# Kernel tuning notes

Hardware: AMD Instinct MI355X
Metric: run time of the kernel (lower is better)

## Reference

```python
import jax, jax.numpy as jnp
import numpy as np

N, E, D, H, L, R = 10000, 48000, 768, 4, 4, 3
NEG = -1e30


def setup_inputs() -> dict:
    key = jax.random.key(0)
    ks = jax.random.split(key, 16)
    s = 0.02
    return {
        'node_features': jax.random.normal(ks[0], (N, D), jnp.float32),
        'edge_index': jax.random.randint(ks[1], (2, E), 0, N, jnp.int64 if jax.config.jax_enable_x64 else jnp.int32),
        'edge_type': jax.random.randint(ks[2], (E,), 0, R, jnp.int64 if jax.config.jax_enable_x64 else jnp.int32),
        'rel_W': jax.random.normal(ks[3], (R, D, D), jnp.float32) * s,
        'rel_b': jnp.zeros((R, D), jnp.float32),
        'gat_W': jax.random.normal(ks[4], (L, D, H * D), jnp.float32) * s,
        'gat_att_src': jax.random.normal(ks[5], (L, H, D), jnp.float32) * s,
        'gat_att_dst': jax.random.normal(ks[6], (L, H, D), jnp.float32) * s,
        'gat_bias': jnp.zeros((L, D), jnp.float32),
        'proj_W1': jax.random.normal(ks[7], (D, 512), jnp.float32) * s,
        'proj_b1': jnp.zeros((512,), jnp.float32),
        'proj_W2': jax.random.normal(ks[8], (512, D), jnp.float32) * s,
        'proj_b2': jnp.zeros((D,), jnp.float32),
    }


def _gat_rel(g, a_src, a_dst, bias, src, dst, emask):
    # g: [N,H,D] transformed per-head node features; PyG GATConv with
    # add_self_loops=True, leaky_relu slope 0.2, concat=False (head mean).
    alpha_s = jnp.einsum('nhd,hd->nh', g, a_src)   # [N,H]
    alpha_d = jnp.einsum('nhd,hd->nh', g, a_dst)   # [N,H]
    e = jax.nn.leaky_relu(alpha_s[src] + alpha_d[dst], 0.2)  # [E,H]
    e = jnp.where(emask[:, None], e, NEG)          # mask other relations
    e_self = jax.nn.leaky_relu(alpha_s + alpha_d, 0.2)       # [N,H] self loops
    m = jax.ops.segment_max(e, dst, num_segments=N)
    m = jnp.maximum(m, e_self)                     # stable softmax max per dst
    p = jnp.where(emask[:, None], jnp.exp(e - m[dst]), 0.0)  # [E,H]
    p_self = jnp.exp(e_self - m)                   # [N,H]
    denom = jax.ops.segment_sum(p, dst, num_segments=N) + p_self
    msg = jax.ops.segment_sum(p[:, :, None] * g[src], dst, num_segments=N)
    msg = msg + p_self[:, :, None] * g             # [N,H,D]
    out = msg / denom[:, :, None]
    return out.mean(axis=1) + bias                 # concat=False -> head mean


def reference(node_features, edge_index, edge_type, rel_W, rel_b, gat_W,
              gat_att_src, gat_att_dst, gat_bias, proj_W1, proj_b1,
              proj_W2, proj_b2):
    src, dst = edge_index[0], edge_index[1]
    h = node_features
    for l in range(L):
        h_new = jnp.zeros_like(h)
        for r in range(R):
            emask = edge_type == r
            t = h @ rel_W[r] + rel_b[r]                    # relation transform
            g = (t @ gat_W[l]).reshape(N, H, D)            # [N,H,D]
            h_new = h_new + _gat_rel(g, gat_att_src[l], gat_att_dst[l],
                                     gat_bias[l], src, dst, emask)
        h = jax.nn.relu(h + h_new)                         # residual + relu
    positions = jax.nn.relu(h @ proj_W1 + proj_b1) @ proj_W2 + proj_b2
    return positions, h
```

## Files before the change

kernel.cpp:

```cpp
#include <hip/hip_runtime.h>
#include <stdint.h>

#define NN 10000
#define NE 48000
#define DIM 768
#define NH 4
#define NL 4
#define NR 3
#define HD 3072
#define NPAD 10240
#define NRD (NR*DIM)
#define SCN (NR*NN)
#define SCB ((SCN+255)/256)

typedef __attribute__((ext_vector_type(8))) short bf16x8;
typedef __attribute__((ext_vector_type(4))) float f32x4;

__device__ __forceinline__ unsigned short f2b(float f){
  union {float f; unsigned u;} v; v.f=f;
  unsigned r = v.u + 0x7FFFu + ((v.u>>16)&1u);
  return (unsigned short)(r>>16);
}
__device__ __forceinline__ float b2f(unsigned short b){
  union {unsigned u; float f;} v; v.u = ((unsigned)b)<<16; return v.f;
}

__device__ __forceinline__ void gl_lds16(const void* g, void* l){
  __builtin_amdgcn_global_load_lds(
    reinterpret_cast<const __attribute__((address_space(1))) uint32_t*>(reinterpret_cast<uintptr_t>(g)),
    reinterpret_cast<__attribute__((address_space(3))) uint32_t*>(reinterpret_cast<uintptr_t>(l)),
    16, 0, 0);
}

#define MPH(P) \
  { _Pragma("unroll") for (int ni=0; ni<NB; ni++) \
      _Pragma("unroll") for (int ks=0; ks<2; ks++) \
        acc[P][ni] = __builtin_amdgcn_mfma_f32_16x16x32_bf16( \
          a[P][ks], b[ni][ks], acc[P][ni],0,0,0); }

template<int MODE>
__global__ __launch_bounds__(512, 4)
void gemmU(const unsigned short* __restrict__ A, const unsigned short* __restrict__ Bt,
           void* __restrict__ C, unsigned short* __restrict__ C2,
           const float* __restrict__ RH, const float* __restrict__ bias, float bscale,
           int K, int Mvalid, int ldc)
{
  constexpr int NB     = 2;
  constexpr int ABYTES = 16384;
  constexpr int SLOT   = 32768;
  __shared__ char lds2[2*SLOT];

  const int tid = threadIdx.x;
  const int lane = tid & 63;
  const int wv = tid >> 6;
  const int wr = wv >> 2;
  const int wc = wv & 3;
  const int fr = lane & 15;
  const int fs = lane >> 4;

  int bx, by;
  {
    int fid = blockIdx.y * gridDim.x + blockIdx.x;
    if ((gridDim.y & 7) == 0){
      int xcd = fid & 7, slot = fid >> 3;
      bx = slot % gridDim.x;
      by = (slot / gridDim.x) * 8 + xcd;
    } else { bx = blockIdx.x; by = blockIdx.y; }
  }

  const unsigned short* Ag = A + (size_t)by * 128 * K;
  const unsigned short* Bg = Bt + (size_t)bx * 128 * K;
  const int T = K >> 6;

  f32x4 acc[4][NB];
  #pragma unroll
  for (int i=0;i<4;i++)
    #pragma unroll
    for (int j=0;j<NB;j++) acc[i][j] = (f32x4){0.f,0.f,0.f,0.f};

  auto stage = [&](int t2, int c){
    char* region = lds2 + (t2 & 1) * SLOT;
    const unsigned short* G = Ag;
    int off = c * 8192 + tid * 16;
    if (c >= 2){ G = Bg; off -= ABYTES; region += ABYTES; }
    int row = off >> 7;
    int srcslot = ((off >> 4) & 7) ^ (row & 7);
    gl_lds16((const char*)(G + (size_t)row * K + (size_t)t2 * 64) + (srcslot << 4),
             region + off);
  };

  #pragma unroll
  for (int c=0;c<4;c++) stage(0,c);
  __builtin_amdgcn_sched_barrier(0);
  stage(1,0); stage(1,1);
  __builtin_amdgcn_sched_barrier(0);

  for (int t=0; t<T; ++t){
    const char* As_ = lds2 + (t&1)*SLOT;
    const char* Bs_ = As_ + ABYTES;

    if (t < T-1) asm volatile("s_waitcnt vmcnt(2)" ::: "memory");
    else         asm volatile("s_waitcnt vmcnt(0)" ::: "memory");
    __builtin_amdgcn_s_barrier();

    bf16x8 a[4][2], b[NB][2];
    #pragma unroll
    for (int mi=0; mi<4; mi++){
      const int row = wr*64 + mi*16 + fr;
      #pragma unroll
      for (int ks=0; ks<2; ks++){
        const int bo = row*128 + ((((ks<<2)+fs) ^ (row&7))<<4);
        a[mi][ks] = *(const bf16x8*)(As_ + bo);
      }
    }
    #pragma unroll
    for (int ni=0; ni<NB; ni++){
      const int row = wc*32 + ni*16 + fr;
      #pragma unroll
      for (int ks=0; ks<2; ks++){
        const int bo = row*128 + ((((ks<<2)+fs) ^ (row&7))<<4);
        b[ni][ks] = *(const bf16x8*)(Bs_ + bo);
      }
    }
    if (t+1 < T){ stage(t+1, 2); stage(t+1, 3); }
    asm volatile("s_waitcnt lgkmcnt(0)" ::: "memory");
    __builtin_amdgcn_s_setprio(1); MPH(0); __builtin_amdgcn_s_setprio(0);
    __builtin_amdgcn_s_barrier();

    if (t+2 < T){ stage(t+2, 0); stage(t+2, 1); }
    __builtin_amdgcn_s_setprio(1); MPH(1); __builtin_amdgcn_s_setprio(0);
    __builtin_amdgcn_s_barrier();

    __builtin_amdgcn_s_setprio(1); MPH(2); __builtin_amdgcn_s_setprio(0);
    __builtin_amdgcn_s_barrier();

    __builtin_amdgcn_s_setprio(1); MPH(3); __builtin_amdgcn_s_setprio(0);
  }

  const int cr = (lane>>4)<<2, cc = lane&15;
  #pragma unroll
  for (int mi=0; mi<4; mi++){
    #pragma unroll
    for (int ni=0; ni<NB; ni++){
      const int col = bx*128 + wc*32 + ni*16 + cc;
      const float bv = bias ? bscale*bias[col] : 0.0f;
      #pragma unroll
      for (int j=0; j<4; j++){
        const int row = by*128 + wr*64 + mi*16 + cr + j;
        if (row < Mvalid){
          const size_t o = (size_t)row*ldc + col;
          float v = acc[mi][ni][j] + bv;
          if (MODE==2) v = v>0.f?v:0.f;
          if (MODE==0)      ((float*)C)[o] = v;
          else if (MODE==1 || MODE==2) ((unsigned short*)C)[o] = f2b(v);
          else {
            float w = RH[o] + v;
            w = w>0.f?w:0.f;
            ((float*)C)[o] = w; C2[o] = f2b(w);
          }
        }
      }
    }
  }
}

__global__ void k_init(const float* __restrict__ nf, float* __restrict__ h, unsigned short* __restrict__ hb){
  for (size_t i = (size_t)blockIdx.x*256+threadIdx.x; i < (size_t)NPAD*DIM; i += (size_t)gridDim.x*256){
    float v = (i < (size_t)NN*DIM) ? nf[i] : 0.0f;
    h[i]=v; hb[i]=f2b(v);
  }
}
__global__ void k_transpose(const float* __restrict__ in, unsigned short* __restrict__ out,
                            int rows, int cols, long in_bs, long out_bs){
  __shared__ float tile[32][33];
  int b = blockIdx.z;
  int r0 = blockIdx.y*32, c0 = blockIdx.x*32;
  int tx = threadIdx.x & 31, ty = threadIdx.x >> 5;
  const float* ip = in + (size_t)b*in_bs;
  unsigned short* op = out + (size_t)b*out_bs;
  #pragma unroll
  for (int i=ty;i<32;i+=8) tile[i][tx] = ip[(size_t)(r0+i)*cols + c0+tx];
  __syncthreads();
  #pragma unroll
  for (int i=ty;i<32;i+=8) op[(size_t)(c0+i)*rows + r0+tx] = f2b(tile[tx][i]);
}
__global__ void k_gatws(const float* __restrict__ gat_W, unsigned short* __restrict__ out){
  __shared__ float tile[32][33];
  int z = blockIdx.z; int l = z>>2, h = z&3;
  size_t base = (size_t)l*DIM*HD + (size_t)h*DIM;
  int r0 = blockIdx.y*32, c0 = blockIdx.x*32;
  int tx = threadIdx.x & 31, ty = threadIdx.x >> 5;
  #pragma unroll
  for (int i=ty;i<32;i+=8) tile[i][tx] = gat_W[base + (size_t)(r0+i)*HD + c0+tx];
  __syncthreads();
  #pragma unroll
  for (int i=ty;i<32;i+=8) out[base + (size_t)(c0+i)*HD + r0+tx] = f2b(0.25f*tile[tx][i]);
}

__global__ __launch_bounds__(256) void k_vsrc(const float* __restrict__ gat_W, const float* __restrict__ a_src,
                       const float* __restrict__ a_dst, float* __restrict__ vs, float* __restrict__ vd){
  int gw = blockIdx.x*4 + (threadIdx.x>>6);
  if (gw >= NL*DIM) return;
  int l = gw/DIM;
  int lane = threadIdx.x & 63;
  const float* grow = gat_W + (size_t)gw*HD;
  #pragma unroll
  for (int h=0;h<NH;h++){
    const float* asr = a_src + ((size_t)l*NH + h)*DIM;
    const float* adr = a_dst + ((size_t)l*NH + h)*DIM;
    float s=0.f,d=0.f;
    for (int dd=lane; dd<DIM; dd+=64){
      float gv = grow[h*DIM+dd];
      s += gv*asr[dd]; d += gv*adr[dd];
    }
    #pragma unroll
    for (int o=32;o>=1;o>>=1){ s += __shfl_xor(s,o,64); d += __shfl_xor(d,o,64); }
    if (lane==0){ vs[(size_t)gw*NH+h]=s; vd[(size_t)gw*NH+h]=d; }
  }
}
__global__ __launch_bounds__(256) void k_wa(const float* __restrict__ rel_W, const float* __restrict__ vs,
                     const float* __restrict__ vd, float* __restrict__ was, float* __restrict__ wad){
  int gw = blockIdx.x*4 + (threadIdx.x>>6);
  if (gw >= NL*NR*DIM) return;
  int lr = gw/DIM, k = gw%DIM;
  int l = lr/NR, r = lr%NR;
  int lane = threadIdx.x & 63;
  const float* wrow = rel_W + ((size_t)r*DIM + k)*DIM;
  float s0=0,s1=0,s2=0,s3=0,d0=0,d1=0,d2=0,d3=0;
  for (int q=lane; q<DIM; q+=64){
    float w = wrow[q];
    const float4 v1 = *(const float4*)(vs + ((size_t)l*DIM+q)*NH);
    const float4 v2 = *(const float4*)(vd + ((size_t)l*DIM+q)*NH);
    s0+=w*v1.x; s1+=w*v1.y; s2+=w*v1.z; s3+=w*v1.w;
    d0+=w*v2.x; d1+=w*v2.y; d2+=w*v2.z; d3+=w*v2.w;
  }
  #pragma unroll
  for (int o=32;o>=1;o>>=1){
    s0+=__shfl_xor(s0,o,64); s1+=__shfl_xor(s1,o,64); s2+=__shfl_xor(s2,o,64); s3+=__shfl_xor(s3,o,64);
    d0+=__shfl_xor(d0,o,64); d1+=__shfl_xor(d1,o,64); d2+=__shfl_xor(d2,o,64); d3+=__shfl_xor(d3,o,64);
  }
  if (lane==0){
    float4* ps = (float4*)(was + (size_t)gw*NH); *ps = make_float4(s0,s1,s2,s3);
    float4* pd = (float4*)(wad + (size_t)gw*NH); *pd = make_float4(d0,d1,d2,d3);
  }
}
__global__ void k_bsd(const float* __restrict__ rel_b, const float* __restrict__ vs, const float* __restrict__ vd,
                      float* __restrict__ bs, float* __restrict__ bd){
  int t = threadIdx.x; if (t >= NL*NR*NH) return;
  int l = t/(NR*NH), r = (t/NH)%NR, h = t%NH;
  float s=0.f,d=0.f;
  for (int q=0;q<DIM;q++){
    float b = rel_b[r*DIM+q];
    s += b*vs[((size_t)l*DIM+q)*NH+h];
    d += b*vd[((size_t)l*DIM+q)*NH+h];
  }
  bs[t]=s; bd[t]=d;
}

__global__ void k_count(const int* __restrict__ et, const int* __restrict__ ei, int* __restrict__ counts){
  int e = blockIdx.x*256+threadIdx.x; if (e>=NE) return;
  atomicAdd(&counts[et[e]*NN + ei[NE+e]], 1);
}
__global__ void k_scan1(const int* __restrict__ counts, int* __restrict__ excl, int* __restrict__ part){
  __shared__ int tmp[256];
  int b = blockIdx.x, t = threadIdx.x, idx = b*256+t;
  int v = (idx<SCN)? counts[idx] : 0;
  tmp[t]=v; __syncthreads();
  #pragma unroll
  for (int off=1; off<256; off<<=1){
    int x = (t>=off)? tmp[t-off] : 0;
    __syncthreads(); tmp[t]+=x; __syncthreads();
  }
  if (idx<SCN) excl[idx] = tmp[t]-v;
  if (t==255) part[b] = tmp[255];
}
__global__ void k_scan2(int* __restrict__ part){
  if (threadIdx.x==0){
    int c=0;
    for (int i=0;i<SCB;i++){ int v=part[i]; part[i]=c; c+=v; }
    part[SCB]=c;
  }
}
__global__ void k_scan3(int* __restrict__ rs, const int* __restrict__ part, int* __restrict__ cursor){
  int b = blockIdx.x, idx = b*256+threadIdx.x;
  if (idx<SCN){
    int e = rs[idx] + part[b];
    rs[idx]=e; cursor[idx]=e;
  }
  if (idx==0) rs[SCN] = part[SCB];
}
__global__ void k_fill(const int* __restrict__ et, const int* __restrict__ ei, int* __restrict__ cursor,
                       int* __restrict__ csrs, int* __restrict__ csre){
  int e = blockIdx.x*256+threadIdx.x; if (e>=NE) return;
  int pos = atomicAdd(&cursor[et[e]*NN + ei[NE+e]], 1);
  csrs[pos] = ei[e];
  csre[pos] = e;
}

__global__ __launch_bounds__(256) void k_alpha(const float* __restrict__ h,
    const float* __restrict__ WAS, const float* __restrict__ WAD,
    const float* __restrict__ BS, const float* __restrict__ BD,
    float* __restrict__ aS, float* __restrict__ aD,
    float* __restrict__ eself, float* __restrict__ mbuf, float* __restrict__ den, int l)
{
  int n = blockIdx.x*4 + (threadIdx.x>>6);
  if (n >= NN) return;
  int lane = threadIdx.x & 63;
  const float* hrow = h + (size_t)n*DIM;
  float hv[12];
  #pragma unroll
  for (int i=0;i<12;i++) hv[i] = hrow[lane + i*64];
  #pragma unroll
  for (int r=0;r<NR;r++){
    const float* was = WAS + ((size_t)(l*NR+r)*DIM)*NH;
    const float* wad = WAD + ((size_t)(l*NR+r)*DIM)*NH;
    float as[NH]={0,0,0,0}, ad[NH]={0,0,0,0};
    #pragma unroll
    for (int i=0;i<12;i++){
      int k = lane + i*64;
      const float4 wsv = *(const float4*)(was + (size_t)k*NH);
      const float4 wdv = *(const float4*)(wad + (size_t)k*NH);
      as[0]+=hv[i]*wsv.x; as[1]+=hv[i]*wsv.y; as[2]+=hv[i]*wsv.z; as[3]+=hv[i]*wsv.w;
      ad[0]+=hv[i]*wdv.x; ad[1]+=hv[i]*wdv.y; ad[2]+=hv[i]*wdv.z; ad[3]+=hv[i]*wdv.w;
    }
    #pragma unroll
    for (int o=32;o>=1;o>>=1){
      #pragma unroll
      for (int hh=0;hh<NH;hh++){
        as[hh] += __shfl_xor(as[hh], o, 64);
        ad[hh] += __shfl_xor(ad[hh], o, 64);
      }
    }
    if (lane==0){
      int rn = r*NN+n;
      #pragma unroll
      for (int hh=0;hh<NH;hh++){
        float A = as[hh]+BS[(l*NR+r)*NH+hh], B = ad[hh]+BD[(l*NR+r)*NH+hh];
        aS[rn*NH+hh]=A; aD[rn*NH+hh]=B;
        float es = A+B; es = es>0.f?es:0.2f*es;
        eself[rn*NH+hh]=es; mbuf[rn*NH+hh]=es; den[rn*NH+hh]=0.f;
      }
    }
  }
}
__device__ __forceinline__ void atomicMaxF(float* addr, float val){
  int* ia = (int*)addr;
  float curf = *((volatile float*)addr);
  while (val > curf){
    int old = atomicCAS(ia, __float_as_int(curf), __float_as_int(val));
    if (old == __float_as_int(curf)) break;
    curf = __int_as_float(old);
  }
}
__global__ void k_edge_max(const int* __restrict__ ei, const int* __restrict__ et,
                           const float* __restrict__ aS, const float* __restrict__ aD,
                           float* __restrict__ mbuf){
  int e = blockIdx.x*256+threadIdx.x; if (e>=NE) return;
  int r = et[e];
  int s = r*NN + ei[e], d = r*NN + ei[NE+e];
  #pragma unroll
  for (int hh=0;hh<NH;hh++){
    float x = aS[s*NH+hh] + aD[d*NH+hh]; x = x>0.f?x:0.2f*x;
    atomicMaxF(&mbuf[d*NH+hh], x);
  }
}
__global__ void k_edge_p(const int* __restrict__ ei, const int* __restrict__ et,
                         const float* __restrict__ aS, const float* __restrict__ aD,
                         const float* __restrict__ mbuf, float* __restrict__ den,
                         float* __restrict__ pbuf){
  int e = blockIdx.x*256+threadIdx.x; if (e>=NE) return;
  int r = et[e];
  int s = r*NN + ei[e], d = r*NN + ei[NE+e];
  #pragma unroll
  for (int hh=0;hh<NH;hh++){
    float x = aS[s*NH+hh] + aD[d*NH+hh]; x = x>0.f?x:0.2f*x;
    float p = __expf(x - mbuf[d*NH+hh]);
    pbuf[e*NH+hh]=p;
    atomicAdd(&den[d*NH+hh], p);
  }
}
__global__ __launch_bounds__(256) void k_aggz(const unsigned short* __restrict__ T3,
    const float* __restrict__ eself, const float* __restrict__ mbuf, const float* __restrict__ den,
    const float* __restrict__ pbuf, const int* __restrict__ row_start,
    const int* __restrict__ csrs, const int* __restrict__ csre,
    unsigned short* __restrict__ Z)
{
  int n = blockIdx.x, t = threadIdx.x;
  float z[3][NH];
  #pragma unroll
  for (int u=0;u<3;u++)
    #pragma unroll
    for (int hh=0;hh<NH;hh++) z[u][hh]=0.f;

  for (int r=0;r<NR;r++){
    int rn = r*NN+n;
    float ps[NH], inv[NH];
    #pragma unroll
    for (int hh=0;hh<NH;hh++){
      float p0 = __expf(eself[rn*NH+hh]-mbuf[rn*NH+hh]);
      ps[hh]=p0; inv[hh]=1.0f/(den[rn*NH+hh]+p0);
    }
    const unsigned short* tn = T3 + (size_t)n*NRD + r*DIM;
    float acc[3][NH];
    #pragma unroll
    for (int u=0;u<3;u++){
      float tv = b2f(tn[t+256*u]);
      #pragma unroll
      for (int hh=0;hh<NH;hh++) acc[u][hh] = ps[hh]*tv;
    }
    int beg = row_start[rn], end = row_start[rn+1];
    for (int p=beg;p<end;p++){
      int s = csrs[p]; int id = csre[p];
      float pe[NH];
      #pragma unroll
      for (int hh=0;hh<NH;hh++) pe[hh]=pbuf[id*NH+hh];
      const unsigned short* ts = T3 + (size_t)s*NRD + r*DIM;
      #pragma unroll
      for (int u=0;u<3;u++){
        float tv = b2f(ts[t+256*u]);
        #pragma unroll
        for (int hh=0;hh<NH;hh++) acc[u][hh] += pe[hh]*tv;
      }
    }
    #pragma unroll
    for (int u=0;u<3;u++)
      #pragma unroll
      for (int hh=0;hh<NH;hh++) z[u][hh] += inv[hh]*acc[u][hh];
  }
  #pragma unroll
  for (int u=0;u<3;u++)
    #pragma unroll
    for (int hh=0;hh<NH;hh++)
      Z[(size_t)n*HD + hh*DIM + t + 256*u] = f2b(z[u][hh]);
}

static constexpr size_t al(size_t x){ return (x + 255) & ~(size_t)255; }
static constexpr size_t OFF_H     = 0;
static constexpr size_t OFF_HB    = OFF_H    + al((size_t)NPAD*DIM*4);
static constexpr size_t OFF_T3    = OFF_HB   + al((size_t)NPAD*DIM*2);
static constexpr size_t OFF_Z     = OFF_T3   + al((size_t)NPAD*NRD*2);
static constexpr size_t OFF_GATWS = OFF_Z    + al((size_t)NPAD*HD*2);
static constexpr size_t OFF_RELWT = OFF_GATWS+ al((size_t)NL*DIM*HD*2);
static constexpr size_t OFF_W1T   = OFF_RELWT+ al((size_t)NR*DIM*DIM*2);
static constexpr size_t OFF_W2T   = OFF_W1T  + al((size_t)512*DIM*2);
static constexpr size_t OFF_ZP    = OFF_W2T  + al((size_t)DIM*512*2);
static constexpr size_t OFF_VS    = OFF_ZP   + al((size_t)NPAD*512*2);
static constexpr size_t OFF_VD    = OFF_VS   + al((size_t)NL*DIM*NH*4);
static constexpr size_t OFF_WAS   = OFF_VD   + al((size_t)NL*DIM*NH*4);
static constexpr size_t OFF_WAD   = OFF_WAS  + al((size_t)NL*NR*DIM*NH*4);
static constexpr size_t OFF_BS    = OFF_WAD  + al((size_t)NL*NR*DIM*NH*4);
static constexpr size_t OFF_BD    = OFF_BS   + al((size_t)NL*NR*NH*4);
static constexpr size_t OFF_AS    = OFF_BD   + al((size_t)NL*NR*NH*4);
static constexpr size_t OFF_AD    = OFF_AS   + al((size_t)SCN*NH*4);
static constexpr size_t OFF_ESELF = OFF_AD   + al((size_t)SCN*NH*4);
static constexpr size_t OFF_M     = OFF_ESELF+ al((size_t)SCN*NH*4);
static constexpr size_t OFF_DEN   = OFF_M    + al((size_t)SCN*NH*4);
static constexpr size_t OFF_PBUF  = OFF_DEN  + al((size_t)SCN*NH*4);
static constexpr size_t OFF_CNT   = OFF_PBUF + al((size_t)NE*NH*4);
static constexpr size_t OFF_RSTART= OFF_CNT  + al((size_t)SCN*4);
static constexpr size_t OFF_PART  = OFF_RSTART+al(((size_t)SCN+1)*4);
static constexpr size_t OFF_CUR   = OFF_PART + al(((size_t)SCB+1)*4);
static constexpr size_t OFF_CSRS  = OFF_CUR  + al((size_t)SCN*4);
static constexpr size_t OFF_CSRE  = OFF_CSRS + al((size_t)NE*4);

extern "C" void kernel_launch(void* const* d_in, const int* in_sizes, int n_in,
                              void* d_out, int out_size, void* d_ws, size_t ws_size,
                              hipStream_t stream) {
  const float* nf     = (const float*)d_in[0];
  const int*   ei     = (const int*)d_in[1];
  const int*   etype  = (const int*)d_in[2];
  const float* rel_W  = (const float*)d_in[3];
  const float* rel_b  = (const float*)d_in[4];
  const float* gat_W  = (const float*)d_in[5];
  const float* a_src  = (const float*)d_in[6];
  const float* a_dst  = (const float*)d_in[7];
  const float* gat_bias=(const float*)d_in[8];
  const float* pW1    = (const float*)d_in[9];
  const float* pb1    = (const float*)d_in[10];
  const float* pW2    = (const float*)d_in[11];
  const float* pb2    = (const float*)d_in[12];
  float* out = (float*)d_out;
  char* ws = (char*)d_ws;

  float*          H     = (float*)(ws+OFF_H);
  unsigned short* HB    = (unsigned short*)(ws+OFF_HB);
  unsigned short* T3    = (unsigned short*)(ws+OFF_T3);
  unsigned short* Z     = (unsigned short*)(ws+OFF_Z);
  unsigned short* GATWS = (unsigned short*)(ws+OFF_GATWS);
  unsigned short* RELWT = (unsigned short*)(ws+OFF_RELWT);
  unsigned short* W1T   = (unsigned short*)(ws+OFF_W1T);
  unsigned short* W2T   = (unsigned short*)(ws+OFF_W2T);
  unsigned short* ZP    = (unsigned short*)(ws+OFF_ZP);
  float* VS   = (float*)(ws+OFF_VS);
  float* VD   = (float*)(ws+OFF_VD);
  float* WAS  = (float*)(ws+OFF_WAS);
  float* WAD  = (float*)(ws+OFF_WAD);
  float* BS   = (float*)(ws+OFF_BS);
  float* BD   = (float*)(ws+OFF_BD);
  float* AS_  = (float*)(ws+OFF_AS);
  float* AD_  = (float*)(ws+OFF_AD);
  float* ESELF= (float*)(ws+OFF_ESELF);
  float* MBUF = (float*)(ws+OFF_M);
  float* DEN  = (float*)(ws+OFF_DEN);
  float* PBUF = (float*)(ws+OFF_PBUF);
  int* COUNTS = (int*)(ws+OFF_CNT);
  int* RSTART = (int*)(ws+OFF_RSTART);
  int* PART   = (int*)(ws+OFF_PART);
  int* CURSOR = (int*)(ws+OFF_CUR);
  int* CSRS   = (int*)(ws+OFF_CSRS);
  int* CSRE   = (int*)(ws+OFF_CSRE);

  k_init<<<2048,256,0,stream>>>(nf, H, HB);
  k_transpose<<<dim3(DIM/32, DIM/32, NR),256,0,stream>>>(rel_W, RELWT, DIM, DIM, (long)DIM*DIM, (long)DIM*DIM);
  k_gatws<<<dim3(DIM/32, DIM/32, NL*NH),256,0,stream>>>(gat_W, GATWS);
  k_transpose<<<dim3(512/32, DIM/32, 1),256,0,stream>>>(pW1, W1T, DIM, 512, 0, 0);
  k_transpose<<<dim3(DIM/32, 512/32, 1),256,0,stream>>>(pW2, W2T, 512, DIM, 0, 0);
  (void)hipMemsetAsync(COUNTS, 0, (size_t)SCN*4, stream);
  k_count<<<(NE+255)/256,256,0,stream>>>(etype, ei, COUNTS);
  k_scan1<<<SCB,256,0,stream>>>(COUNTS, RSTART, PART);
  k_scan2<<<1,64,0,stream>>>(PART);
  k_scan3<<<SCB,256,0,stream>>>(RSTART, PART, CURSOR);
  k_fill<<<(NE+255)/256,256,0,stream>>>(etype, ei, CURSOR, CSRS, CSRE);
  k_vsrc<<<NL*DIM/4,256,0,stream>>>(gat_W, a_src, a_dst, VS, VD);
  k_wa<<<NL*NR*DIM/4,256,0,stream>>>(rel_W, VS, VD, WAS, WAD);
  k_bsd<<<1,64,0,stream>>>(rel_b, VS, VD, BS, BD);

  for (int l=0; l<NL; l++){
    gemmU<1><<<dim3(NRD/128, NPAD/128),512,0,stream>>>(
        HB, RELWT, T3, nullptr, nullptr, rel_b, 1.0f, DIM, NN, NRD);
    k_alpha<<<(NN+3)/4,256,0,stream>>>(H, WAS, WAD, BS, BD, AS_, AD_, ESELF, MBUF, DEN, l);
    k_edge_max<<<(NE+255)/256,256,0,stream>>>(ei, etype, AS_, AD_, MBUF);
    k_edge_p<<<(NE+255)/256,256,0,stream>>>(ei, etype, AS_, AD_, MBUF, DEN, PBUF);
    k_aggz<<<NN,256,0,stream>>>(T3, ESELF, MBUF, DEN, PBUF, RSTART, CSRS, CSRE, Z);
    float* hw = (l==NL-1) ? (out + (size_t)NN*DIM) : H;
    gemmU<3><<<dim3(DIM/128, NPAD/128),512,0,stream>>>(
        Z, GATWS + (size_t)l*DIM*HD, hw, HB, H, gat_bias + (size_t)l*DIM, 3.0f, HD, NN, DIM);
  }

  gemmU<2><<<dim3(512/128, NPAD/128),512,0,stream>>>(
      HB, W1T, ZP, nullptr, nullptr, pb1, 1.0f, DIM, NN, 512);
  gemmU<0><<<dim3(DIM/128, NPAD/128),512,0,stream>>>(
      ZP, W2T, out, nullptr, nullptr, pb2, 1.0f, 512, NN, DIM);
}
```

Measured before the change: 962.1 us.

## Switch GEMM to 4-wave blocks with 64x64 per-wave tiles

Rewrites the bf16 MFMA GEMM to use 256-thread blocks (4 waves in a 2x2 grid), each wave computing a 64x64 output tile instead of 64x32 with 8 waves. Each thread now stages twice as many global-to-LDS loads per K step. The MFMA phases are regrouped into two halves, and a split lgkmcnt wait lets the first half start before all LDS reads finish. This is meant to raise register-level reuse of the A/B fragments and cut LDS read traffic per MFMA, at the cost of more accumulator registers, lower occupancy and fewer barriers to hide load latency.

```diff
diff --git a/kernel.cpp b/kernel.cpp
--- a/kernel.cpp
+++ b/kernel.cpp
@@ -32,20 +32,20 @@
     16, 0, 0);
 }
 
-#define MPH(P) \
-  { _Pragma("unroll") for (int ni=0; ni<NB; ni++) \
-      _Pragma("unroll") for (int ks=0; ks<2; ks++) \
-        acc[P][ni] = __builtin_amdgcn_mfma_f32_16x16x32_bf16( \
-          a[P][ks], b[ni][ks], acc[P][ni],0,0,0); }
+#define MPH2(P) \
+  { _Pragma("unroll") for (int mi=2*(P); mi<2*(P)+2; mi++) \
+      _Pragma("unroll") for (int ni=0; ni<4; ni++) \
+        _Pragma("unroll") for (int ks=0; ks<2; ks++) \
+          acc[mi][ni] = __builtin_amdgcn_mfma_f32_16x16x32_bf16( \
+            a[mi][ks], b[ni][ks], acc[mi][ni],0,0,0); }
 
 template<int MODE>
-__global__ __launch_bounds__(512, 4)
-void gemmU(const unsigned short* __restrict__ A, const unsigned short* __restrict__ Bt,
+__global__ __launch_bounds__(256, 2)
+void gemmV(const unsigned short* __restrict__ A, const unsigned short* __restrict__ Bt,
            void* __restrict__ C, unsigned short* __restrict__ C2,
            const float* __restrict__ RH, const float* __restrict__ bias, float bscale,
            int K, int Mvalid, int ldc)
 {
-  constexpr int NB     = 2;
   constexpr int ABYTES = 16384;
   constexpr int SLOT   = 32768;
   __shared__ char lds2[2*SLOT];
@@ -53,8 +53,8 @@
   const int tid = threadIdx.x;
   const int lane = tid & 63;
   const int wv = tid >> 6;
-  const int wr = wv >> 2;
-  const int wc = wv & 3;
+  const int wr = wv >> 1;
+  const int wc = wv & 1;
   const int fr = lane & 15;
   const int fs = lane >> 4;
 
@@ -72,17 +72,17 @@
   const unsigned short* Bg = Bt + (size_t)bx * 128 * K;
   const int T = K >> 6;
 
-  f32x4 acc[4][NB];
+  f32x4 acc[4][4];
   #pragma unroll
   for (int i=0;i<4;i++)
     #pragma unroll
-    for (int j=0;j<NB;j++) acc[i][j] = (f32x4){0.f,0.f,0.f,0.f};
+    for (int j=0;j<4;j++) acc[i][j] = (f32x4){0.f,0.f,0.f,0.f};
 
   auto stage = [&](int t2, int c){
     char* region = lds2 + (t2 & 1) * SLOT;
     const unsigned short* G = Ag;
-    int off = c * 8192 + tid * 16;
-    if (c >= 2){ G = Bg; off -= ABYTES; region += ABYTES; }
+    int off = c * 4096 + tid * 16;
+    if (c >= 4){ G = Bg; off -= ABYTES; region += ABYTES; }
     int row = off >> 7;
     int srcslot = ((off >> 4) & 7) ^ (row & 7);
     gl_lds16((const char*)(G + (size_t)row * K + (size_t)t2 * 64) + (srcslot << 4),
@@ -90,20 +90,30 @@
   };
 
   #pragma unroll
-  for (int c=0;c<4;c++) stage(0,c);
+  for (int c=0;c<8;c++) stage(0,c);
   __builtin_amdgcn_sched_barrier(0);
-  stage(1,0); stage(1,1);
+  #pragma unroll
+  for (int c=0;c<4;c++) stage(1,c);
   __builtin_amdgcn_sched_barrier(0);
 
   for (int t=0; t<T; ++t){
     const char* As_ = lds2 + (t&1)*SLOT;
     const char* Bs_ = As_ + ABYTES;
 
-    if (t < T-1) asm volatile("s_waitcnt vmcnt(2)" ::: "memory");
+    if (t < T-1) asm volatile("s_waitcnt vmcnt(4)" ::: "memory");
     else         asm volatile("s_waitcnt vmcnt(0)" ::: "memory");
     __builtin_amdgcn_s_barrier();
 
-    bf16x8 a[4][2], b[NB][2];
+    bf16x8 a[4][2], b[4][2];
+    #pragma unroll
+    for (int ni=0; ni<4; ni++){
+      const int row = wc*64 + ni*16 + fr;
+      #pragma unroll
+      for (int ks=0; ks<2; ks++){
+        const int bo = row*128 + ((((ks<<2)+fs) ^ (row&7))<<4);
+        b[ni][ks] = *(const bf16x8*)(Bs_ + bo);
+      }
+    }
     #pragma unroll
     for (int mi=0; mi<4; mi++){
       const int row = wr*64 + mi*16 + fr;
@@ -113,36 +123,25 @@
         a[mi][ks] = *(const bf16x8*)(As_ + bo);
       }
     }
-    #pragma unroll
-    for (int ni=0; ni<NB; ni++){
-      const int row = wc*32 + ni*16 + fr;
-      #pragma unroll
-      for (int ks=0; ks<2; ks++){
-        const int bo = row*128 + ((((ks<<2)+fs) ^ (row&7))<<4);
-        b[ni][ks] = *(const bf16x8*)(Bs_ + bo);
-      }
-    }
-    if (t+1 < T){ stage(t+1, 2); stage(t+1, 3); }
+    if (t+1 < T){ stage(t+1,4); stage(t+1,5); stage(t+1,6); stage(t+1,7); }
+    asm volatile("s_waitcnt lgkmcnt(4)" ::: "memory");
+    __builtin_amdgcn_sched_barrier(0);
+    __builtin_amdgcn_s_setprio(1); MPH2(0); __builtin_amdgcn_s_setprio(0);
     asm volatile("s_waitcnt lgkmcnt(0)" ::: "memory");
-    __builtin_amdgcn_s_setprio(1); MPH(0); __builtin_amdgcn_s_setprio(0);
+    __builtin_amdgcn_sched_barrier(0);
+    __builtin_amdgcn_s_setprio(1); MPH2(1); __builtin_amdgcn_s_setprio(0);
     __builtin_amdgcn_s_barrier();
 
-    if (t+2 < T){ stage(t+2, 0); stage(t+2, 1); }
-    __builtin_amdgcn_s_setprio(1); MPH(1); __builtin_amdgcn_s_setprio(0);
-    __builtin_amdgcn_s_barrier();
-
-    __builtin_amdgcn_s_setprio(1); MPH(2); __builtin_amdgcn_s_setprio(0);
-    __builtin_amdgcn_s_barrier();
-
-    __builtin_amdgcn_s_setprio(1); MPH(3); __builtin_amdgcn_s_setprio(0);
+    if (t+2 < T){ stage(t+2,0); stage(t+2,1); stage(t+2,2); stage(t+2,3); }
+    __builtin_amdgcn_s_setprio(1); MPH2(2); MPH2(3); __builtin_amdgcn_s_setprio(0);
   }
 
   const int cr = (lane>>4)<<2, cc = lane&15;
   #pragma unroll
   for (int mi=0; mi<4; mi++){
     #pragma unroll
-    for (int ni=0; ni<NB; ni++){
-      const int col = bx*128 + wc*32 + ni*16 + cc;
+    for (int ni=0; ni<4; ni++){
+      const int col = bx*128 + wc*64 + ni*16 + cc;
       const float bv = bias ? bscale*bias[col] : 0.0f;
       #pragma unroll
       for (int j=0; j<4; j++){
@@ -526,19 +525,19 @@
   k_bsd<<<1,64,0,stream>>>(rel_b, VS, VD, BS, BD);
 
   for (int l=0; l<NL; l++){
-    gemmU<1><<<dim3(NRD/128, NPAD/128),512,0,stream>>>(
+    gemmV<1><<<dim3(NRD/128, NPAD/128),256,0,stream>>>(
         HB, RELWT, T3, nullptr, nullptr, rel_b, 1.0f, DIM, NN, NRD);
     k_alpha<<<(NN+3)/4,256,0,stream>>>(H, WAS, WAD, BS, BD, AS_, AD_, ESELF, MBUF, DEN, l);
     k_edge_max<<<(NE+255)/256,256,0,stream>>>(ei, etype, AS_, AD_, MBUF);
     k_edge_p<<<(NE+255)/256,256,0,stream>>>(ei, etype, AS_, AD_, MBUF, DEN, PBUF);
     k_aggz<<<NN,256,0,stream>>>(T3, ESELF, MBUF, DEN, PBUF, RSTART, CSRS, CSRE, Z);
     float* hw = (l==NL-1) ? (out + (size_t)NN*DIM) : H;
-    gemmU<3><<<dim3(DIM/128, NPAD/128),512,0,stream>>>(
+    gemmV<3><<<dim3(DIM/128, NPAD/128),256,0,stream>>>(
         Z, GATWS + (size_t)l*DIM*HD, hw, HB, H, gat_bias + (size_t)l*DIM, 3.0f, HD, NN, DIM);
   }
 
-  gemmU<2><<<dim3(512/128, NPAD/128),512,0,stream>>>(
+  gemmV<2><<<dim3(512/128, NPAD/128),256,0,stream>>>(
       HB, W1T, ZP, nullptr, nullptr, pb1, 1.0f, DIM, NN, 512);
-  gemmU<0><<<dim3(DIM/128, NPAD/128),512,0,stream>>>(
+  gemmV<0><<<dim3(DIM/128, NPAD/128),256,0,stream>>>(
       ZP, W2T, out, nullptr, nullptr, pb2, 1.0f, 512, NN, DIM);
 }
```

New measurement: 1.014 ms. +5.4%, slower.

## Fuse edge softmax into CSR aggregation and simplify GEMM main loop schedule

Applied to the files above, without the earlier changes.

Removes the separate edge-max and edge-p kernels, which used global float atomics (CAS max and atomicAdd), and recomputes the per-destination softmax max, exponentials and denominator inside the CSR aggregation kernel by walking each row twice. This drops the eself, mbuf, den and pbuf buffers and two launches per layer, at the cost of redundant exp and alpha reads per block. Separately, the GEMM inner loop now loads all LDS fragments, waits and barriers once, issues the next prefetch stages, then runs all MFMAs in one block instead of interleaving four MFMA phases with barriers. That reduces the number of barriers but may overlap global loads with compute less well.

```diff
diff --git a/kernel.cpp b/kernel.cpp
--- a/kernel.cpp
+++ b/kernel.cpp
@@ -32,12 +32,6 @@
     16, 0, 0);
 }
 
-#define MPH(P) \
-  { _Pragma("unroll") for (int ni=0; ni<NB; ni++) \
-      _Pragma("unroll") for (int ks=0; ks<2; ks++) \
-        acc[P][ni] = __builtin_amdgcn_mfma_f32_16x16x32_bf16( \
-          a[P][ks], b[ni][ks], acc[P][ni],0,0,0); }
-
 template<int MODE>
 __global__ __launch_bounds__(512, 4)
 void gemmU(const unsigned short* __restrict__ A, const unsigned short* __restrict__ Bt,
@@ -105,6 +99,15 @@
 
     bf16x8 a[4][2], b[NB][2];
     #pragma unroll
+    for (int ni=0; ni<NB; ni++){
+      const int row = wc*32 + ni*16 + fr;
+      #pragma unroll
+      for (int ks=0; ks<2; ks++){
+        const int bo = row*128 + ((((ks<<2)+fs) ^ (row&7))<<4);
+        b[ni][ks] = *(const bf16x8*)(Bs_ + bo);
+      }
+    }
+    #pragma unroll
     for (int mi=0; mi<4; mi++){
       const int row = wr*64 + mi*16 + fr;
       #pragma unroll
@@ -113,28 +116,23 @@
         a[mi][ks] = *(const bf16x8*)(As_ + bo);
       }
     }
-    #pragma unroll
-    for (int ni=0; ni<NB; ni++){
-      const int row = wc*32 + ni*16 + fr;
-      #pragma unroll
-      for (int ks=0; ks<2; ks++){
-        const int bo = row*128 + ((((ks<<2)+fs) ^ (row&7))<<4);
-        b[ni][ks] = *(const bf16x8*)(Bs_ + bo);
-      }
-    }
+    asm volatile("s_waitcnt lgkmcnt(0)" ::: "memory");
+    __builtin_amdgcn_s_barrier();
+
     if (t+1 < T){ stage(t+1, 2); stage(t+1, 3); }
-    asm volatile("s_waitcnt lgkmcnt(0)" ::: "memory");
-    __builtin_amdgcn_s_setprio(1); MPH(0); __builtin_amdgcn_s_setprio(0);
-    __builtin_amdgcn_s_barrier();
-
     if (t+2 < T){ stage(t+2, 0); stage(t+2, 1); }
-    __builtin_amdgcn_s_setprio(1); MPH(1); __builtin_amdgcn_s_setprio(0);
-    __builtin_amdgcn_s_barrier();
-
-    __builtin_amdgcn_s_setprio(1); MPH(2); __builtin_amdgcn_s_setprio(0);
-    __builtin_amdgcn_s_barrier();
-
-    __builtin_amdgcn_s_setprio(1); MPH(3); __builtin_amdgcn_s_setprio(0);
+    __builtin_amdgcn_sched_barrier(0);
+
+    __builtin_amdgcn_s_setprio(1);
+    #pragma unroll
+    for (int mi=0; mi<4; mi++)
+      #pragma unroll
+      for (int ni=0; ni<NB; ni++)
+        #pragma unroll
+        for (int ks=0; ks<2; ks++)
+          acc[mi][ni] = __builtin_amdgcn_mfma_f32_16x16x32_bf16(
+              a[mi][ks], b[ni][ks], acc[mi][ni], 0,0,0);
+    __builtin_amdgcn_s_setprio(0);
   }
 
   const int cr = (lane>>4)<<2, cc = lane&15;
@@ -300,8 +298,7 @@
 __global__ __launch_bounds__(256) void k_alpha(const float* __restrict__ h,
     const float* __restrict__ WAS, const float* __restrict__ WAD,
     const float* __restrict__ BS, const float* __restrict__ BD,
-    float* __restrict__ aS, float* __restrict__ aD,
-    float* __restrict__ eself, float* __restrict__ mbuf, float* __restrict__ den, int l)
+    float* __restrict__ aS, float* __restrict__ aD, int l)
 {
   int n = blockIdx.x*4 + (threadIdx.x>>6);
   if (n >= NN) return;
@@ -335,54 +332,16 @@
       int rn = r*NN+n;
       #pragma unroll
       for (int hh=0;hh<NH;hh++){
-        float A = as[hh]+BS[(l*NR+r)*NH+hh], B = ad[hh]+BD[(l*NR+r)*NH+hh];
-        aS[rn*NH+hh]=A; aD[rn*NH+hh]=B;
-        float es = A+B; es = es>0.f?es:0.2f*es;
-        eself[rn*NH+hh]=es; mbuf[rn*NH+hh]=es; den[rn*NH+hh]=0.f;
-      }
-    }
-  }
-}
-__device__ __forceinline__ void atomicMaxF(float* addr, float val){
-  int* ia = (int*)addr;
-  float curf = *((volatile float*)addr);
-  while (val > curf){
-    int old = atomicCAS(ia, __float_as_int(curf), __float_as_int(val));
-    if (old == __float_as_int(curf)) break;
-    curf = __int_as_float(old);
-  }
-}
-__global__ void k_edge_max(const int* __restrict__ ei, const int* __restrict__ et,
-                           const float* __restrict__ aS, const float* __restrict__ aD,
-                           float* __restrict__ mbuf){
-  int e = blockIdx.x*256+threadIdx.x; if (e>=NE) return;
-  int r = et[e];
-  int s = r*NN + ei[e], d = r*NN + ei[NE+e];
-  #pragma unroll
-  for (int hh=0;hh<NH;hh++){
-    float x = aS[s*NH+hh] + aD[d*NH+hh]; x = x>0.f?x:0.2f*x;
-    atomicMaxF(&mbuf[d*NH+hh], x);
-  }
-}
-__global__ void k_edge_p(const int* __restrict__ ei, const int* __restrict__ et,
-                         const float* __restrict__ aS, const float* __restrict__ aD,
-                         const float* __restrict__ mbuf, float* __restrict__ den,
-                         float* __restrict__ pbuf){
-  int e = blockIdx.x*256+threadIdx.x; if (e>=NE) return;
-  int r = et[e];
-  int s = r*NN + ei[e], d = r*NN + ei[NE+e];
-  #pragma unroll
-  for (int hh=0;hh<NH;hh++){
-    float x = aS[s*NH+hh] + aD[d*NH+hh]; x = x>0.f?x:0.2f*x;
-    float p = __expf(x - mbuf[d*NH+hh]);
-    pbuf[e*NH+hh]=p;
-    atomicAdd(&den[d*NH+hh], p);
-  }
-}
+        aS[rn*NH+hh] = as[hh]+BS[(l*NR+r)*NH+hh];
+        aD[rn*NH+hh] = ad[hh]+BD[(l*NR+r)*NH+hh];
+      }
+    }
+  }
+}
+
 __global__ __launch_bounds__(256) void k_aggz(const unsigned short* __restrict__ T3,
-    const float* __restrict__ eself, const float* __restrict__ mbuf, const float* __restrict__ den,
-    const float* __restrict__ pbuf, const int* __restrict__ row_start,
-    const int* __restrict__ csrs, const int* __restrict__ csre,
+    const float* __restrict__ aS, const float* __restrict__ aD,
+    const int* __restrict__ row_start, const int* __restrict__ csrs,
     unsigned short* __restrict__ Z)
 {
   int n = blockIdx.x, t = threadIdx.x;
@@ -394,26 +353,52 @@
 
   for (int r=0;r<NR;r++){
     int rn = r*NN+n;
-    float ps[NH], inv[NH];
-    #pragma unroll
-    for (int hh=0;hh<NH;hh++){
-      float p0 = __expf(eself[rn*NH+hh]-mbuf[rn*NH+hh]);
-      ps[hh]=p0; inv[hh]=1.0f/(den[rn*NH+hh]+p0);
-    }
-    const unsigned short* tn = T3 + (size_t)n*NRD + r*DIM;
-    float acc[3][NH];
-    #pragma unroll
-    for (int u=0;u<3;u++){
-      float tv = b2f(tn[t+256*u]);
-      #pragma unroll
-      for (int hh=0;hh<NH;hh++) acc[u][hh] = ps[hh]*tv;
+    const float4 adv = *(const float4*)(aD + (size_t)rn*NH);
+    const float4 asv = *(const float4*)(aS + (size_t)rn*NH);
+    const float ad_n[NH] = {adv.x, adv.y, adv.z, adv.w};
+    float es[NH], m[NH];
+    {
+      const float as_n[NH] = {asv.x, asv.y, asv.z, asv.w};
+      #pragma unroll
+      for (int hh=0;hh<NH;hh++){
+        float e = as_n[hh] + ad_n[hh]; e = e>0.f?e:0.2f*e;
+        es[hh]=e; m[hh]=e;
+      }
     }
     int beg = row_start[rn], end = row_start[rn+1];
     for (int p=beg;p<end;p++){
-      int s = csrs[p]; int id = csre[p];
+      int s = csrs[p];
+      const float4 av = *(const float4*)(aS + ((size_t)r*NN+s)*NH);
+      const float ash[NH] = {av.x, av.y, av.z, av.w};
+      #pragma unroll
+      for (int hh=0;hh<NH;hh++){
+        float e = ash[hh] + ad_n[hh]; e = e>0.f?e:0.2f*e;
+        m[hh] = fmaxf(m[hh], e);
+      }
+    }
+    float den[NH], acc[3][NH];
+    const unsigned short* tn = T3 + (size_t)n*NRD + r*DIM;
+    {
+      float ps[NH];
+      #pragma unroll
+      for (int hh=0;hh<NH;hh++){ ps[hh]=__expf(es[hh]-m[hh]); den[hh]=ps[hh]; }
+      #pragma unroll
+      for (int u=0;u<3;u++){
+        float tv = b2f(tn[t+256*u]);
+        #pragma unroll
+        for (int hh=0;hh<NH;hh++) acc[u][hh] = ps[hh]*tv;
+      }
+    }
+    for (int p=beg;p<end;p++){
+      int s = csrs[p];
+      const float4 av = *(const float4*)(aS + ((size_t)r*NN+s)*NH);
+      const float ash[NH] = {av.x, av.y, av.z, av.w};
       float pe[NH];
       #pragma unroll
-      for (int hh=0;hh<NH;hh++) pe[hh]=pbuf[id*NH+hh];
+      for (int hh=0;hh<NH;hh++){
+        float e = ash[hh] + ad_n[hh]; e = e>0.f?e:0.2f*e;
+        pe[hh] = __expf(e - m[hh]); den[hh] += pe[hh];
+      }
       const unsigned short* ts = T3 + (size_t)s*NRD + r*DIM;
       #pragma unroll
       for (int u=0;u<3;u++){
@@ -423,9 +408,11 @@
       }
     }
     #pragma unroll
-    for (int u=0;u<3;u++)
-      #pragma unroll
-      for (int hh=0;hh<NH;hh++) z[u][hh] += inv[hh]*acc[u][hh];
+    for (int hh=0;hh<NH;hh++){
+      float inv = 1.0f/den[hh];
+      #pragma unroll
+      for (int u=0;u<3;u++) z[u][hh] += inv*acc[u][hh];
+    }
   }
   #pragma unroll
   for (int u=0;u<3;u++)
@@ -452,11 +439,7 @@
 static constexpr size_t OFF_BD    = OFF_BS   + al((size_t)NL*NR*NH*4);
 static constexpr size_t OFF_AS    = OFF_BD   + al((size_t)NL*NR*NH*4);
 static constexpr size_t OFF_AD    = OFF_AS   + al((size_t)SCN*NH*4);
-static constexpr size_t OFF_ESELF = OFF_AD   + al((size_t)SCN*NH*4);
-static constexpr size_t OFF_M     = OFF_ESELF+ al((size_t)SCN*NH*4);
-static constexpr size_t OFF_DEN   = OFF_M    + al((size_t)SCN*NH*4);
-static constexpr size_t OFF_PBUF  = OFF_DEN  + al((size_t)SCN*NH*4);
-static constexpr size_t OFF_CNT   = OFF_PBUF + al((size_t)NE*NH*4);
+static constexpr size_t OFF_CNT   = OFF_AD   + al((size_t)SCN*NH*4);
 static constexpr size_t OFF_RSTART= OFF_CNT  + al((size_t)SCN*4);
 static constexpr size_t OFF_PART  = OFF_RSTART+al(((size_t)SCN+1)*4);
 static constexpr size_t OFF_CUR   = OFF_PART + al(((size_t)SCB+1)*4);
@@ -499,10 +482,6 @@
   float* BD   = (float*)(ws+OFF_BD);
   float* AS_  = (float*)(ws+OFF_AS);
   float* AD_  = (float*)(ws+OFF_AD);
-  float* ESELF= (float*)(ws+OFF_ESELF);
-  float* MBUF = (float*)(ws+OFF_M);
-  float* DEN  = (float*)(ws+OFF_DEN);
-  float* PBUF = (float*)(ws+OFF_PBUF);
   int* COUNTS = (int*)(ws+OFF_CNT);
   int* RSTART = (int*)(ws+OFF_RSTART);
   int* PART   = (int*)(ws+OFF_PART);
@@ -528,10 +507,8 @@
   for (int l=0; l<NL; l++){
     gemmU<1><<<dim3(NRD/128, NPAD/128),512,0,stream>>>(
         HB, RELWT, T3, nullptr, nullptr, rel_b, 1.0f, DIM, NN, NRD);
-    k_alpha<<<(NN+3)/4,256,0,stream>>>(H, WAS, WAD, BS, BD, AS_, AD_, ESELF, MBUF, DEN, l);
-    k_edge_max<<<(NE+255)/256,256,0,stream>>>(ei, etype, AS_, AD_, MBUF);
-    k_edge_p<<<(NE+255)/256,256,0,stream>>>(ei, etype, AS_, AD_, MBUF, DEN, PBUF);
-    k_aggz<<<NN,256,0,stream>>>(T3, ESELF, MBUF, DEN, PBUF, RSTART, CSRS, CSRE, Z);
+    k_alpha<<<(NN+3)/4,256,0,stream>>>(H, WAS, WAD, BS, BD, AS_, AD_, l);
+    k_aggz<<<NN,256,0,stream>>>(T3, AS_, AD_, RSTART, CSRS, Z);
     float* hw = (l==NL-1) ? (out + (size_t)NN*DIM) : H;
     gemmU<3><<<dim3(DIM/128, NPAD/128),512,0,stream>>>(
         Z, GATWS + (size_t)l*DIM*HD, hw, HB, H, gat_bias + (size_t)l*DIM, 3.0f, HD, NN, DIM);
```

New measurement: 890.0 us. -7.5%, faster.
